# Kernel optimization log

Hardware: AMD Instinct MI355X
Metric: run time of the kernel (lower is better)

Reference implementation:

```python
import jax, jax.numpy as jnp
import numpy as np

EPS = 1e-06

def elu_feature_map(x):
    return jax.nn.elu(x) + 1.0

def setup_inputs() -> dict:
    key = jax.random.key(0)
    kq, kk, kv = jax.random.split(key, 3)
    shape = (4, 8, 4096, 64)  # [B, H, L, D]
    return {
        "queries": jax.random.normal(kq, shape, dtype=jnp.float32),
        "keys": jax.random.normal(kk, shape, dtype=jnp.float32),
        "values": jax.random.normal(kv, shape, dtype=jnp.float32),
    }

def reference(queries, keys, values):
    Q = elu_feature_map(queries)            # [b,h,l,d]
    K = elu_feature_map(keys)               # [b,h,l,d]
    v_length = values.shape[-2]
    values_n = values / v_length            # [b,h,l,v]
    KV = jnp.einsum('bhld,bhlv->bhdv', K, values_n)          # [b,h,d,v]
    Z = 1.0 / (jnp.einsum('bhld,bhd->bhl', Q, K.sum(axis=-2)) + EPS)  # [b,h,l]
    out = jnp.einsum('bhld,bhdv,bhl->bhlv', Q, KV, Z) * v_length
    return out
```

## Files before the change

kernel.cpp:

```cpp
#include <hip/hip_runtime.h>


#define LSEQ   4096
#define DDIM   64
#define NHEAD  32
#define K1CH   32
#define K1ROWS (LSEQ / K1CH)
#define T1ROWS 16
#define NT1    (K1ROWS / T1ROWS)
#define WSPH   (DDIM * DDIM + DDIM)
#define WSPH4  (WSPH / 4)
#define ST2    84

typedef float f2 __attribute__((ext_vector_type(2)));

__device__ __forceinline__ float fmap(float x) {
    return x > 0.0f ? (x + 1.0f) : __expf(x);
}
__device__ __forceinline__ float4 fmap4(float4 v) {
    v.x = fmap(v.x); v.y = fmap(v.y); v.z = fmap(v.z); v.w = fmap(v.w);
    return v;
}
__device__ __forceinline__ f2 pkfma(f2 a, f2 b, f2 c) {
    return __builtin_elementwise_fma(a, b, c);
}

__global__ __launch_bounds__(256) void la_kv_kernel(
    const float* __restrict__ Kg, const float* __restrict__ Vg,
    float* __restrict__ ws)
{
    __shared__ float kst[2][T1ROWS * DDIM];
    __shared__ float vst[2][T1ROWS * DDIM];
    __shared__ float red[DDIM * DDIM];
    __shared__ float kred[DDIM];

    const int t    = threadIdx.x;
    const int wave = t >> 6;
    const int lane = t & 63;
    const int dq   = lane >> 3;
    const int vq   = lane & 7;

    const int bh    = blockIdx.x / K1CH;
    const int chunk = blockIdx.x % K1CH;
    const size_t base = (size_t)bh * LSEQ * DDIM + (size_t)chunk * K1ROWS * DDIM;
    const float4* Kb4 = (const float4*)(Kg + base);
    const float4* Vb4 = (const float4*)(Vg + base);

    ((float4*)kst[0])[t] = fmap4(Kb4[t]);
    ((float4*)vst[0])[t] = Vb4[t];
    __syncthreads();

    f2 acc[8][4];
    f2 ksum2[4] = {(f2)(0.f), (f2)(0.f), (f2)(0.f), (f2)(0.f)};
#pragma unroll
    for (int i = 0; i < 8; ++i)
#pragma unroll
        for (int j = 0; j < 4; ++j) acc[i][j] = (f2)(0.0f);

#pragma unroll 1
    for (int tl = 0; tl < NT1; ++tl) {
        const int cur = tl & 1;
        const bool pre = (tl + 1 < NT1);
        float4 kx, vx;
        if (pre) {
            kx = Kb4[(tl + 1) * 256 + t];
            vx = Vb4[(tl + 1) * 256 + t];
        }

#pragma unroll
        for (int r = 0; r < 4; ++r) {
            const int l = wave * 4 + r;
            const float4 ka = *(const float4*)(kst[cur] + l * DDIM + dq * 8);
            const float4 kb = *(const float4*)(kst[cur] + l * DDIM + dq * 8 + 4);
            const float4 va = *(const float4*)(vst[cur] + l * DDIM + vq * 4);
            const float4 vb = *(const float4*)(vst[cur] + l * DDIM + 32 + vq * 4);
            const float kk[8] = {ka.x, ka.y, ka.z, ka.w, kb.x, kb.y, kb.z, kb.w};
            const f2 vv[4] = {{va.x, va.y}, {va.z, va.w}, {vb.x, vb.y}, {vb.z, vb.w}};
            ksum2[0] += (f2){kk[0], kk[1]};
            ksum2[1] += (f2){kk[2], kk[3]};
            ksum2[2] += (f2){kk[4], kk[5]};
            ksum2[3] += (f2){kk[6], kk[7]};
#pragma unroll
            for (int i = 0; i < 8; ++i) {
                const f2 ki = {kk[i], kk[i]};
#pragma unroll
                for (int j = 0; j < 4; ++j)
                    acc[i][j] = pkfma(ki, vv[j], acc[i][j]);
            }
        }

        if (pre) {
            ((float4*)kst[cur ^ 1])[t] = fmap4(kx);
            ((float4*)vst[cur ^ 1])[t] = vx;
        }
        __syncthreads();
    }

    float4* red4 = (float4*)red;
    for (int w = 0; w < 4; ++w) {
        __syncthreads();
        if (wave == w) {
            const int pj = vq ^ dq;
#pragma unroll
            for (int i = 0; i < 8; ++i) {
                const int d = dq * 8 + i;
                float4 lo = make_float4(acc[i][0].x, acc[i][0].y, acc[i][1].x, acc[i][1].y);
                float4 hi = make_float4(acc[i][2].x, acc[i][2].y, acc[i][3].x, acc[i][3].y);
                float4* plo = red4 + d * 16 + pj;
                float4* phi = red4 + d * 16 + 8 + pj;
                if (w != 0) {
                    const float4 a = *plo; const float4 b = *phi;
                    lo.x += a.x; lo.y += a.y; lo.z += a.z; lo.w += a.w;
                    hi.x += b.x; hi.y += b.y; hi.z += b.z; hi.w += b.w;
                }
                *plo = lo; *phi = hi;
            }
            if (vq == 0) {
                float* p = kred + dq * 8;
#pragma unroll
                for (int j = 0; j < 4; ++j) {
                    f2 s = ksum2[j];
                    if (w != 0) { s.x += p[2*j]; s.y += p[2*j+1]; }
                    p[2*j] = s.x; p[2*j+1] = s.y;
                }
            }
        }
    }
    __syncthreads();

    float4* dst = (float4*)(ws + (size_t)blockIdx.x * WSPH);
    for (int i = t; i < 1024; i += 256) {
        const int row = i >> 4, j = i & 15;
        const int pj = (((j & 7) ^ (row >> 3)) | (j & 8));
        dst[i] = red4[row * 16 + pj];
    }
    if (t < 16)
        dst[1024 + t] = ((const float4*)kred)[t];
}

__global__ __launch_bounds__(256) void la_reduce_kernel(
    const float* __restrict__ ws, float* __restrict__ kvout)
{
    const int h   = blockIdx.x / 5;
    const int seg = blockIdx.x % 5;
    const int t   = threadIdx.x;
    if (t >= 208) return;
    const int i4 = seg * 208 + t;

    const float4* base = (const float4*)(ws + (size_t)h * K1CH * WSPH) + i4;
    float4 acc = make_float4(0.f, 0.f, 0.f, 0.f);
#pragma unroll 8
    for (int p = 0; p < K1CH; ++p) {
        const float4 x = base[(size_t)p * WSPH4];
        acc.x += x.x; acc.y += x.y; acc.z += x.z; acc.w += x.w;
    }
    ((float4*)(kvout + (size_t)h * WSPH))[i4] = acc;
}

__global__ __launch_bounds__(256) void la_out_kernel(
    const float* __restrict__ Qg, const float* __restrict__ kvin,
    float* __restrict__ out)
{
    __shared__ float qlds[128 * ST2];
    __shared__ float kvlds[DDIM * DDIM];
    __shared__ float ksl[DDIM];
    __shared__ float zs[128];

    const int t    = threadIdx.x;
    const int bh   = blockIdx.x >> 5;
    const int tile = blockIdx.x & 31;
    const size_t base = (size_t)bh * LSEQ * DDIM + (size_t)tile * 128 * DDIM;
    const float4* Qb4 = (const float4*)(Qg + base);

#pragma unroll
    for (int i = 0; i < 8; ++i) {
        const int o = t + i * 256;
        const float4 q = fmap4(Qb4[o]);
        const int row = o >> 4, c4 = o & 15;
        *(float4*)(qlds + row * ST2 + c4 * 4) = q;
    }
    const float4* wsrc = (const float4*)(kvin + (size_t)bh * WSPH);
    for (int i = t; i < WSPH4; i += 256) {
        const float4 x = wsrc[i];
        if (i < 1024) ((float4*)kvlds)[i] = x;
        else          ((float4*)ksl)[i - 1024] = x;
    }
    __syncthreads();

    {
        const int row  = t >> 1;
        const int half = t & 1;
        float s = 0.0f;
#pragma unroll
        for (int j = 0; j < 8; ++j) {
            const float4 q  = *(const float4*)(qlds + row * ST2 + half * 32 + j * 4);
            const float4 ks = *(const float4*)(ksl + half * 32 + j * 4);
            s += q.x * ks.x + q.y * ks.y + q.z * ks.z + q.w * ks.w;
        }
        s += __shfl_xor(s, 1);
        if (half == 0) zs[row] = 1.0f / (s + 1e-6f);
    }
    __syncthreads();

    const int rg = t >> 3;
    const int vq = t & 7;
    f2 acc[4][4];
#pragma unroll
    for (int k = 0; k < 4; ++k)
#pragma unroll
        for (int j = 0; j < 4; ++j) acc[k][j] = (f2)(0.0f);

#pragma unroll 1
    for (int d4 = 0; d4 < 16; ++d4) {
        f2 kv[4][4];
#pragma unroll
        for (int i = 0; i < 4; ++i) {
            const float4 a = *(const float4*)(kvlds + (d4 * 4 + i) * DDIM + vq * 4);
            const float4 b = *(const float4*)(kvlds + (d4 * 4 + i) * DDIM + 32 + vq * 4);
            kv[i][0] = (f2){a.x, a.y}; kv[i][1] = (f2){a.z, a.w};
            kv[i][2] = (f2){b.x, b.y}; kv[i][3] = (f2){b.z, b.w};
        }
#pragma unroll
        for (int k = 0; k < 4; ++k) {
            const float4 q = *(const float4*)(qlds + (rg + 32 * k) * ST2 + d4 * 4);
            const float qa[4] = {q.x, q.y, q.z, q.w};
#pragma unroll
            for (int i = 0; i < 4; ++i) {
                const f2 qd = {qa[i], qa[i]};
#pragma unroll
                for (int j = 0; j < 4; ++j)
                    acc[k][j] = pkfma(qd, kv[i][j], acc[k][j]);
            }
        }
    }

#pragma unroll
    for (int k = 0; k < 4; ++k) {
        const int row = rg + 32 * k;
        const float z = zs[row];
        float* orow = out + base + (size_t)row * DDIM;
        const float4 lo = make_float4(acc[k][0].x * z, acc[k][0].y * z,
                                      acc[k][1].x * z, acc[k][1].y * z);
        const float4 hi = make_float4(acc[k][2].x * z, acc[k][2].y * z,
                                      acc[k][3].x * z, acc[k][3].y * z);
        *(float4*)(orow + vq * 4) = lo;
        *(float4*)(orow + 32 + vq * 4) = hi;
    }
}

extern "C" void kernel_launch(void* const* d_in, const int* in_sizes, int n_in,
                              void* d_out, int out_size, void* d_ws, size_t ws_size,
                              hipStream_t stream) {
    const float* q = (const float*)d_in[0];
    const float* k = (const float*)d_in[1];
    const float* v = (const float*)d_in[2];
    float* o  = (float*)d_out;
    float* ws = (float*)d_ws;
    float* kvfinal = ws + (size_t)NHEAD * K1CH * WSPH;

    hipLaunchKernelGGL(la_kv_kernel, dim3(NHEAD * K1CH), dim3(256), 0, stream,
                       k, v, ws);
    hipLaunchKernelGGL(la_reduce_kernel, dim3(NHEAD * 5), dim3(256), 0, stream,
                       ws, kvfinal);
    hipLaunchKernelGGL(la_out_kernel, dim3(NHEAD * 32), dim3(256), 0, stream,
                       q, kvfinal, o);
}
```

Baseline: 59.06 us.

## Stream Q from registers in output kernel and enlarge KV staging tiles

The output kernel no longer stages Q through shared memory. Each thread loads 8 rows of Q directly from global memory with software double-buffering, computes the normalizer dot product inline, and handles 256 rows per block, so the grid is halved. The KV kernel stages 32-row tiles instead of 16 and aliases its reduction buffers into one shared array. The aim is to cut LDS traffic, barriers and total block count. In exchange, register pressure in the output kernel rises, and Q is now read with strided global loads rather than coalesced row reads.

Measured after the change: 69.85 us. 18.3% more time.

```diff
diff --git a/kernel.cpp b/kernel.cpp
--- a/kernel.cpp
+++ b/kernel.cpp
@@ -6,11 +6,10 @@
 #define NHEAD  32
 #define K1CH   32
 #define K1ROWS (LSEQ / K1CH)
-#define T1ROWS 16
+#define T1ROWS 32
 #define NT1    (K1ROWS / T1ROWS)
 #define WSPH   (DDIM * DDIM + DDIM)
 #define WSPH4  (WSPH / 4)
-#define ST2    84
 
 typedef float f2 __attribute__((ext_vector_type(2)));
 
@@ -29,10 +28,7 @@
     const float* __restrict__ Kg, const float* __restrict__ Vg,
     float* __restrict__ ws)
 {
-    __shared__ float kst[2][T1ROWS * DDIM];
-    __shared__ float vst[2][T1ROWS * DDIM];
-    __shared__ float red[DDIM * DDIM];
-    __shared__ float kred[DDIM];
+    __shared__ float smem[8192];
 
     const int t    = threadIdx.x;
     const int wave = t >> 6;
@@ -46,8 +42,14 @@
     const float4* Kb4 = (const float4*)(Kg + base);
     const float4* Vb4 = (const float4*)(Vg + base);
 
-    ((float4*)kst[0])[t] = fmap4(Kb4[t]);
-    ((float4*)vst[0])[t] = Vb4[t];
+    {
+        const float4 ka = Kb4[t], kb = Kb4[t + 256];
+        const float4 va = Vb4[t], vb = Vb4[t + 256];
+        ((float4*)smem)[t]       = fmap4(ka);
+        ((float4*)smem)[t + 256] = fmap4(kb);
+        ((float4*)(smem + 4096))[t]       = va;
+        ((float4*)(smem + 4096))[t + 256] = vb;
+    }
     __syncthreads();
 
     f2 acc[8][4];
@@ -61,21 +63,25 @@
     for (int tl = 0; tl < NT1; ++tl) {
         const int cur = tl & 1;
         const bool pre = (tl + 1 < NT1);
-        float4 kx, vx;
+        float4 ka, kb, va, vb;
         if (pre) {
-            kx = Kb4[(tl + 1) * 256 + t];
-            vx = Vb4[(tl + 1) * 256 + t];
-        }
-
-#pragma unroll
-        for (int r = 0; r < 4; ++r) {
-            const int l = wave * 4 + r;
-            const float4 ka = *(const float4*)(kst[cur] + l * DDIM + dq * 8);
-            const float4 kb = *(const float4*)(kst[cur] + l * DDIM + dq * 8 + 4);
-            const float4 va = *(const float4*)(vst[cur] + l * DDIM + vq * 4);
-            const float4 vb = *(const float4*)(vst[cur] + l * DDIM + 32 + vq * 4);
-            const float kk[8] = {ka.x, ka.y, ka.z, ka.w, kb.x, kb.y, kb.z, kb.w};
-            const f2 vv[4] = {{va.x, va.y}, {va.z, va.w}, {vb.x, vb.y}, {vb.z, vb.w}};
+            ka = Kb4[(tl + 1) * 512 + t];
+            kb = Kb4[(tl + 1) * 512 + t + 256];
+            va = Vb4[(tl + 1) * 512 + t];
+            vb = Vb4[(tl + 1) * 512 + t + 256];
+        }
+
+        const float* kc = smem + cur * 2048;
+        const float* vc = smem + 4096 + cur * 2048;
+#pragma unroll
+        for (int r = 0; r < 8; ++r) {
+            const int l = wave * 8 + r;
+            const float4 k0 = *(const float4*)(kc + l * DDIM + dq * 8);
+            const float4 k1 = *(const float4*)(kc + l * DDIM + dq * 8 + 4);
+            const float4 v0 = *(const float4*)(vc + l * DDIM + vq * 4);
+            const float4 v1 = *(const float4*)(vc + l * DDIM + 32 + vq * 4);
+            const float kk[8] = {k0.x, k0.y, k0.z, k0.w, k1.x, k1.y, k1.z, k1.w};
+            const f2 vv[4] = {{v0.x, v0.y}, {v0.z, v0.w}, {v1.x, v1.y}, {v1.z, v1.w}};
             ksum2[0] += (f2){kk[0], kk[1]};
             ksum2[1] += (f2){kk[2], kk[3]};
             ksum2[2] += (f2){kk[4], kk[5]};
@@ -90,13 +96,18 @@
         }
 
         if (pre) {
-            ((float4*)kst[cur ^ 1])[t] = fmap4(kx);
-            ((float4*)vst[cur ^ 1])[t] = vx;
+            float* kn = smem + (cur ^ 1) * 2048;
+            float* vn = smem + 4096 + (cur ^ 1) * 2048;
+            ((float4*)kn)[t]       = fmap4(ka);
+            ((float4*)kn)[t + 256] = fmap4(kb);
+            ((float4*)vn)[t]       = va;
+            ((float4*)vn)[t + 256] = vb;
         }
         __syncthreads();
     }
 
-    float4* red4 = (float4*)red;
+    float4* red4 = (float4*)smem;
+    float*  kred = smem + 4096;
     for (int w = 0; w < 4; ++w) {
         __syncthreads();
         if (wave == w) {
@@ -161,24 +172,22 @@
     const float* __restrict__ Qg, const float* __restrict__ kvin,
     float* __restrict__ out)
 {
-    __shared__ float qlds[128 * ST2];
     __shared__ float kvlds[DDIM * DDIM];
     __shared__ float ksl[DDIM];
-    __shared__ float zs[128];
 
     const int t    = threadIdx.x;
-    const int bh   = blockIdx.x >> 5;
-    const int tile = blockIdx.x & 31;
-    const size_t base = (size_t)bh * LSEQ * DDIM + (size_t)tile * 128 * DDIM;
-    const float4* Qb4 = (const float4*)(Qg + base);
-
-#pragma unroll
-    for (int i = 0; i < 8; ++i) {
-        const int o = t + i * 256;
-        const float4 q = fmap4(Qb4[o]);
-        const int row = o >> 4, c4 = o & 15;
-        *(float4*)(qlds + row * ST2 + c4 * 4) = q;
-    }
+    const int wave = t >> 6;
+    const int lane = t & 63;
+    const int rg   = lane >> 3;
+    const int vq   = lane & 7;
+
+    const int bh   = blockIdx.x >> 4;
+    const int tile = blockIdx.x & 15;
+    const size_t base = (size_t)bh * LSEQ * DDIM + (size_t)tile * 256 * DDIM;
+    const int row0 = wave * 64 + rg * 8;
+    const float4* Qr4 = (const float4*)(Qg + base + (size_t)row0 * DDIM);
+    float* Ob = out + base + (size_t)row0 * DDIM;
+
     const float4* wsrc = (const float4*)(kvin + (size_t)bh * WSPH);
     for (int i = t; i < WSPH4; i += 256) {
         const float4 x = wsrc[i];
@@ -187,64 +196,72 @@
     }
     __syncthreads();
 
-    {
-        const int row  = t >> 1;
-        const int half = t & 1;
-        float s = 0.0f;
-#pragma unroll
-        for (int j = 0; j < 8; ++j) {
-            const float4 q  = *(const float4*)(qlds + row * ST2 + half * 32 + j * 4);
-            const float4 ks = *(const float4*)(ksl + half * 32 + j * 4);
-            s += q.x * ks.x + q.y * ks.y + q.z * ks.z + q.w * ks.w;
-        }
-        s += __shfl_xor(s, 1);
-        if (half == 0) zs[row] = 1.0f / (s + 1e-6f);
-    }
-    __syncthreads();
-
-    const int rg = t >> 3;
-    const int vq = t & 7;
-    f2 acc[4][4];
-#pragma unroll
-    for (int k = 0; k < 4; ++k)
-#pragma unroll
-        for (int j = 0; j < 4; ++j) acc[k][j] = (f2)(0.0f);
+    f2 acc[8][4];
+    f2 den2[8];
+#pragma unroll
+    for (int r = 0; r < 8; ++r) {
+        den2[r] = (f2)(0.0f);
+#pragma unroll
+        for (int j = 0; j < 4; ++j) acc[r][j] = (f2)(0.0f);
+    }
+
+    float4 qA[8], qB[8];
+#pragma unroll
+    for (int r = 0; r < 8; ++r) qA[r] = Qr4[r * 16 + 0];
+
+#define K2_BODY(QBUF, D4)                                                     \
+    {                                                                         \
+        const int dd4 = (D4);                                                 \
+        f2 kv[4][4];                                                          \
+        _Pragma("unroll")                                                     \
+        for (int i = 0; i < 4; ++i) {                                         \
+            const float4 a = *(const float4*)(kvlds + (dd4*4+i)*DDIM + vq*8); \
+            const float4 b = *(const float4*)(kvlds + (dd4*4+i)*DDIM + vq*8+4);\
+            kv[i][0] = (f2){a.x, a.y}; kv[i][1] = (f2){a.z, a.w};             \
+            kv[i][2] = (f2){b.x, b.y}; kv[i][3] = (f2){b.z, b.w};             \
+        }                                                                     \
+        const float4 ks4 = *(const float4*)(ksl + dd4 * 4);                   \
+        const f2 ksa = {ks4.x, ks4.y}, ksb = {ks4.z, ks4.w};                  \
+        _Pragma("unroll")                                                     \
+        for (int r = 0; r < 8; ++r) {                                         \
+            const float4 qf = fmap4(QBUF[r]);                                 \
+            den2[r] = pkfma((f2){qf.x, qf.y}, ksa, den2[r]);                  \
+            den2[r] = pkfma((f2){qf.z, qf.w}, ksb, den2[r]);                  \
+            const float qa[4] = {qf.x, qf.y, qf.z, qf.w};                     \
+            _Pragma("unroll")                                                 \
+            for (int i = 0; i < 4; ++i) {                                     \
+                const f2 qd = {qa[i], qa[i]};                                 \
+                _Pragma("unroll")                                             \
+                for (int j = 0; j < 4; ++j)                                   \
+                    acc[r][j] = pkfma(qd, kv[i][j], acc[r][j]);               \
+            }                                                                 \
+        }                                                                     \
+    }
 
 #pragma unroll 1
-    for (int d4 = 0; d4 < 16; ++d4) {
-        f2 kv[4][4];
-#pragma unroll
-        for (int i = 0; i < 4; ++i) {
-            const float4 a = *(const float4*)(kvlds + (d4 * 4 + i) * DDIM + vq * 4);
-            const float4 b = *(const float4*)(kvlds + (d4 * 4 + i) * DDIM + 32 + vq * 4);
-            kv[i][0] = (f2){a.x, a.y}; kv[i][1] = (f2){a.z, a.w};
-            kv[i][2] = (f2){b.x, b.y}; kv[i][3] = (f2){b.z, b.w};
-        }
-#pragma unroll
-        for (int k = 0; k < 4; ++k) {
-            const float4 q = *(const float4*)(qlds + (rg + 32 * k) * ST2 + d4 * 4);
-            const float qa[4] = {q.x, q.y, q.z, q.w};
-#pragma unroll
-            for (int i = 0; i < 4; ++i) {
-                const f2 qd = {qa[i], qa[i]};
-#pragma unroll
-                for (int j = 0; j < 4; ++j)
-                    acc[k][j] = pkfma(qd, kv[i][j], acc[k][j]);
-            }
-        }
-    }
-
-#pragma unroll
-    for (int k = 0; k < 4; ++k) {
-        const int row = rg + 32 * k;
-        const float z = zs[row];
-        float* orow = out + base + (size_t)row * DDIM;
-        const float4 lo = make_float4(acc[k][0].x * z, acc[k][0].y * z,
-                                      acc[k][1].x * z, acc[k][1].y * z);
-        const float4 hi = make_float4(acc[k][2].x * z, acc[k][2].y * z,
-                                      acc[k][3].x * z, acc[k][3].y * z);
-        *(float4*)(orow + vq * 4) = lo;
-        *(float4*)(orow + 32 + vq * 4) = hi;
+    for (int d4 = 0; d4 < 16; d4 += 2) {
+#pragma unroll
+        for (int r = 0; r < 8; ++r) qB[r] = Qr4[r * 16 + (d4 + 1)];
+        K2_BODY(qA, d4)
+        if (d4 + 2 < 16) {
+#pragma unroll
+            for (int r = 0; r < 8; ++r) qA[r] = Qr4[r * 16 + (d4 + 2)];
+        }
+        K2_BODY(qB, d4 + 1)
+    }
+#undef K2_BODY
+
+#pragma unroll
+    for (int r = 0; r < 8; ++r) {
+        const float den = den2[r].x + den2[r].y;
+        const float z = 1.0f / (den + 1e-6f);
+        float* orow = Ob + r * DDIM + vq * 8;
+        const float4 lo = make_float4(acc[r][0].x * z, acc[r][0].y * z,
+                                      acc[r][1].x * z, acc[r][1].y * z);
+        const float4 hi = make_float4(acc[r][2].x * z, acc[r][2].y * z,
+                                      acc[r][3].x * z, acc[r][3].y * z);
+        *(float4*)(orow)     = lo;
+        *(float4*)(orow + 4) = hi;
     }
 }
 
@@ -262,6 +279,6 @@
                        k, v, ws);
     hipLaunchKernelGGL(la_reduce_kernel, dim3(NHEAD * 5), dim3(256), 0, stream,
                        ws, kvfinal);
-    hipLaunchKernelGGL(la_out_kernel, dim3(NHEAD * 32), dim3(256), 0, stream,
+    hipLaunchKernelGGL(la_out_kernel, dim3(NHEAD * 16), dim3(256), 0, stream,
                        q, kvfinal, o);
 }
```
